# Kernel optimization log

Hardware: AMD Instinct MI355X
Metric: run time of the kernel (lower is better)

## Reference

```python
import jax, jax.numpy as jnp
import numpy as np

N_NODES = 100000
N_EDGES = 1600000
IN_DIM = 64
HID = 128
N_CLASSES = 1
N_GRAPHS = 512


def _glorot(key, shape):
    fan_in, fan_out = shape[0], shape[1]
    lim = (6.0 / (fan_in + fan_out)) ** 0.5
    return jax.random.uniform(key, shape, jnp.float32, -lim, lim)


def setup_inputs() -> dict:
    key = jax.random.key(0)
    ks = jax.random.split(key, 10)
    x = jax.random.normal(ks[0], (N_NODES, IN_DIM), jnp.float32)
    edge_src = jax.random.randint(ks[1], (N_EDGES,), 0, N_NODES)
    edge_dst = jax.random.randint(ks[2], (N_EDGES,), 0, N_NODES)
    graph_ids = jnp.sort(jax.random.randint(ks[3], (N_NODES,), 0, N_GRAPHS))
    return {
        "x": x,
        "edge_src": edge_src,
        "edge_dst": edge_dst,
        "graph_ids": graph_ids,
        "W1": _glorot(ks[4], (IN_DIM, HID)),
        "b1": jnp.zeros((HID,), jnp.float32),
        "W2": _glorot(ks[5], (HID, HID)),
        "b2": jnp.zeros((HID,), jnp.float32),
        "Wc1": _glorot(ks[6], (HID, HID)),
        "bc1": jnp.zeros((HID,), jnp.float32),
        "Wc2": _glorot(ks[7], (HID, HID)),
        "bc2": jnp.zeros((HID,), jnp.float32),
        "Wc3": _glorot(ks[8], (HID, N_CLASSES)),
        "bc3": jnp.zeros((N_CLASSES,), jnp.float32),
    }


def _graph_conv(h, edge_src, edge_dst, W, b):
    # DGL GraphConv, norm='both': out = D_out^{-1/2} A D_in^{-1/2} h W + b
    ones = jnp.ones((edge_src.shape[0],), h.dtype)
    deg_out = jnp.clip(jax.ops.segment_sum(ones, edge_src, num_segments=N_NODES), 1.0)
    deg_in = jnp.clip(jax.ops.segment_sum(ones, edge_dst, num_segments=N_NODES), 1.0)
    h = h * jax.lax.rsqrt(deg_out)[:, None]           # src-side norm
    agg = jax.ops.segment_sum(h[edge_src], edge_dst, num_segments=N_NODES)  # [N, D]
    agg = agg * jax.lax.rsqrt(deg_in)[:, None]        # dst-side norm
    return agg @ W + b


def reference(x, edge_src, edge_dst, graph_ids, W1, b1, W2, b2, Wc1, bc1, Wc2, bc2, Wc3, bc3):
    h = jax.nn.relu(_graph_conv(x, edge_src, edge_dst, W1, b1))
    h = jax.nn.relu(_graph_conv(h, edge_src, edge_dst, W2, b2))
    # mean_nodes pooling over batched graphs
    sums = jax.ops.segment_sum(h, graph_ids, num_segments=N_GRAPHS)  # [G, H]
    cnts = jax.ops.segment_sum(jnp.ones((N_NODES,), h.dtype), graph_ids, num_segments=N_GRAPHS)
    hg = sums / jnp.clip(cnts, 1.0)[:, None]
    out = jax.nn.relu(hg @ Wc1 + bc1)
    out = jax.nn.relu(out @ Wc2 + bc2)
    return out @ Wc3 + bc3  # [G, n_classes]
```

## Files before the change

### kernel.cpp

```cpp
#include <hip/hip_runtime.h>

#define N_NODES 100000
#define N_EDGES 1600000
#define IN_DIM 64
#define HID 128
#define N_GRAPHS 512
#define NBUCK 391

__global__ __launch_bounds__(256) void k_bhist(const int* __restrict__ src, const int* __restrict__ dst,
                                               int* __restrict__ dcnt, int* __restrict__ scnt) {
    __shared__ int hd[NBUCK];
    __shared__ int hs[NBUCK];
    const int t = threadIdx.x;
    const int e0 = blockIdx.x * 4096 + t * 16;
    for (int i = t; i < NBUCK; i += 256) { hd[i] = 0; hs[i] = 0; }
    __syncthreads();
    if (e0 < N_EDGES) {
        const int4* d4 = (const int4*)(dst + e0);
        const int4* s4 = (const int4*)(src + e0);
#pragma unroll
        for (int u = 0; u < 4; ++u) {
            int4 d = d4[u], s = s4[u];
            atomicAdd(&hd[d.x >> 8], 1); atomicAdd(&hd[d.y >> 8], 1);
            atomicAdd(&hd[d.z >> 8], 1); atomicAdd(&hd[d.w >> 8], 1);
            atomicAdd(&hs[s.x >> 8], 1); atomicAdd(&hs[s.y >> 8], 1);
            atomicAdd(&hs[s.z >> 8], 1); atomicAdd(&hs[s.w >> 8], 1);
        }
    }
    __syncthreads();
    for (int i = t; i < NBUCK; i += 256) {
        if (hd[i]) atomicAdd(&dcnt[i], hd[i]);
        if (hs[i]) atomicAdd(&scnt[i], hs[i]);
    }
}

__global__ __launch_bounds__(512) void k_bscan3(const int* __restrict__ dcnt, const int* __restrict__ scnt,
                                                const int* __restrict__ gid,
                                                int* __restrict__ dbase, int* __restrict__ sbase,
                                                int* __restrict__ dcur, int* __restrict__ scur,
                                                int* __restrict__ gstart) {
    const int t = threadIdx.x;
    if (blockIdx.x == 2) {
        for (int g = t; g <= N_GRAPHS; g += 512) {
            int lo = 0, hi = N_NODES;
            while (lo < hi) {
                int mid = (lo + hi) >> 1;
                if (gid[mid] < g) lo = mid + 1; else hi = mid;
            }
            gstart[g] = lo;
        }
        return;
    }
    __shared__ int l[512];
    const int* cntp = (blockIdx.x == 0) ? dcnt : scnt;
    int* basep = (blockIdx.x == 0) ? dbase : sbase;
    int* curp  = (blockIdx.x == 0) ? dcur  : scur;
    int v = (t < NBUCK) ? cntp[t] : 0;
    l[t] = v;
    __syncthreads();
    for (int off = 1; off < 512; off <<= 1) {
        int x = (t >= off) ? l[t - off] : 0;
        __syncthreads();
        l[t] += x;
        __syncthreads();
    }
    if (t < NBUCK) {
        int excl = l[t] - v;
        basep[t] = excl; curp[t] = excl;
    }
    if (t == NBUCK - 1) basep[NBUCK] = l[t];
}

__global__ __launch_bounds__(256) void k_bin2(const int* __restrict__ src, const int* __restrict__ dst,
                                              int* __restrict__ dcur, int* __restrict__ scur,
                                              int* __restrict__ binnedD, int* __restrict__ binnedS) {
    __shared__ int hd[NBUCK];
    __shared__ int bd[NBUCK];
    __shared__ int hs[NBUCK];
    __shared__ int bs[NBUCK];
    const int t = threadIdx.x;
    const int e0 = blockIdx.x * 4096 + t * 16;
    for (int i = t; i < NBUCK; i += 256) { hd[i] = 0; hs[i] = 0; }
    __syncthreads();
    if (e0 < N_EDGES) {
        const int4* d4 = (const int4*)(dst + e0);
        const int4* s4 = (const int4*)(src + e0);
#pragma unroll
        for (int u = 0; u < 4; ++u) {
            int4 d = d4[u], s = s4[u];
            atomicAdd(&hd[d.x >> 8], 1); atomicAdd(&hd[d.y >> 8], 1);
            atomicAdd(&hd[d.z >> 8], 1); atomicAdd(&hd[d.w >> 8], 1);
            atomicAdd(&hs[s.x >> 8], 1); atomicAdd(&hs[s.y >> 8], 1);
            atomicAdd(&hs[s.z >> 8], 1); atomicAdd(&hs[s.w >> 8], 1);
        }
    }
    __syncthreads();
    for (int i = t; i < NBUCK; i += 256) {
        int c = hd[i];
        bd[i] = c ? atomicAdd(&dcur[i], c) : 0;
        hd[i] = 0;
        c = hs[i];
        bs[i] = c ? atomicAdd(&scur[i], c) : 0;
        hs[i] = 0;
    }
    __syncthreads();
    if (e0 < N_EDGES) {
        const int4* d4 = (const int4*)(dst + e0);
        const int4* s4 = (const int4*)(src + e0);
#pragma unroll
        for (int u = 0; u < 4; ++u) {
            int4 d = d4[u];
            int4 s = s4[u];
            int bk, r;
            bk = d.x >> 8; r = atomicAdd(&hd[bk], 1); binnedD[bd[bk] + r] = s.x | ((d.x & 255) << 17);
            bk = d.y >> 8; r = atomicAdd(&hd[bk], 1); binnedD[bd[bk] + r] = s.y | ((d.y & 255) << 17);
            bk = d.z >> 8; r = atomicAdd(&hd[bk], 1); binnedD[bd[bk] + r] = s.z | ((d.z & 255) << 17);
            bk = d.w >> 8; r = atomicAdd(&hd[bk], 1); binnedD[bd[bk] + r] = s.w | ((d.w & 255) << 17);
            bk = s.x >> 8; r = atomicAdd(&hs[bk], 1); binnedS[bs[bk] + r] = s.x;
            bk = s.y >> 8; r = atomicAdd(&hs[bk], 1); binnedS[bs[bk] + r] = s.y;
            bk = s.z >> 8; r = atomicAdd(&hs[bk], 1); binnedS[bs[bk] + r] = s.z;
            bk = s.w >> 8; r = atomicAdd(&hs[bk], 1); binnedS[bs[bk] + r] = s.w;
        }
    }
}

__global__ __launch_bounds__(256) void k_prep2(const int* __restrict__ dbase, const int* __restrict__ sbase,
                                               const int* __restrict__ binnedD, const int* __restrict__ binnedS,
                                               int* __restrict__ rowp, float* __restrict__ rsi,
                                               float* __restrict__ rso, int* __restrict__ col) {
    const int t = threadIdx.x;
    if (blockIdx.x < NBUCK) {
        const int b = blockIdx.x;
        const int n0 = b * 256;
        __shared__ int cnt[256];
        __shared__ int scn[256];
        __shared__ int cur[256];
        __shared__ int sb[2];
        if (t < 2) sb[t] = dbase[b + t];
        cnt[t] = 0;
        __syncthreads();
        const int s = sb[0], e = sb[1];
        for (int i = s + t; i < e; i += 256) atomicAdd(&cnt[binnedD[i] >> 17], 1);
        __syncthreads();
        const int c = cnt[t];
        scn[t] = c;
        __syncthreads();
        for (int off = 1; off < 256; off <<= 1) {
            int v = (t >= off) ? scn[t - off] : 0;
            __syncthreads();
            scn[t] += v;
            __syncthreads();
        }
        const int excl = scn[t] - c;
        cur[t] = excl;
        if (n0 + t < N_NODES) {
            rowp[n0 + t] = s + excl;
            rsi[n0 + t] = 1.0f / sqrtf(fmaxf((float)c, 1.0f));
        }
        if (b == NBUCK - 1 && t == 0) rowp[N_NODES] = e;
        __syncthreads();
        for (int i = s + t; i < e; i += 256) {
            int p = binnedD[i];
            int r = atomicAdd(&cur[p >> 17], 1);
            col[s + r] = p & 0x1FFFF;
        }
    } else {
        const int b = blockIdx.x - NBUCK;
        const int n0 = b * 256;
        __shared__ int cnt2[256];
        __shared__ int sb2[2];
        if (t < 2) sb2[t] = sbase[b + t];
        cnt2[t] = 0;
        __syncthreads();
        const int s = sb2[0], e = sb2[1];
        for (int i = s + t; i < e; i += 256) atomicAdd(&cnt2[binnedS[i] - n0], 1);
        __syncthreads();
        if (n0 + t < N_NODES) rso[n0 + t] = 1.0f / sqrtf(fmaxf((float)cnt2[t], 1.0f));
    }
}

__global__ __launch_bounds__(512, 8) void k_g64mm(const float4* __restrict__ x4, const float* __restrict__ rso,
                                                  const int* __restrict__ rowp, const int* __restrict__ col,
                                                  const float* __restrict__ W, const float* __restrict__ bias,
                                                  const float* __restrict__ rsi, float* __restrict__ out) {
    __shared__ float aggL[32][IN_DIM];
    __shared__ float WL[32 * 128];
    const int t = threadIdx.x;
    const int wid = t >> 6, lane = t & 63;
    const int n0 = blockIdx.x * 32;

    const int grp = lane >> 4, li = lane & 15;
#pragma unroll 1
    for (int it = 0; it < 4; ++it) {
        const int node = n0 + wid * 4 + it;
        const int s = rowp[node], e = rowp[node + 1];
        float ax = 0.f, ay = 0.f, az = 0.f, aw = 0.f;
        int i = s + grp;
        for (; i + 12 < e; i += 16) {
            int c0 = col[i], c1 = col[i + 4], c2 = col[i + 8], c3 = col[i + 12];
            float4 v0 = x4[c0 * 16 + li];
            float4 v1 = x4[c1 * 16 + li];
            float4 v2 = x4[c2 * 16 + li];
            float4 v3 = x4[c3 * 16 + li];
            float r0 = rso[c0], r1 = rso[c1], r2 = rso[c2], r3 = rso[c3];
            ax = fmaf(r0, v0.x, ax); ay = fmaf(r0, v0.y, ay); az = fmaf(r0, v0.z, az); aw = fmaf(r0, v0.w, aw);
            ax = fmaf(r1, v1.x, ax); ay = fmaf(r1, v1.y, ay); az = fmaf(r1, v1.z, az); aw = fmaf(r1, v1.w, aw);
            ax = fmaf(r2, v2.x, ax); ay = fmaf(r2, v2.y, ay); az = fmaf(r2, v2.z, az); aw = fmaf(r2, v2.w, aw);
            ax = fmaf(r3, v3.x, ax); ay = fmaf(r3, v3.y, ay); az = fmaf(r3, v3.z, az); aw = fmaf(r3, v3.w, aw);
        }
        for (; i + 4 < e; i += 8) {
            int c0 = col[i], c1 = col[i + 4];
            float4 v0 = x4[c0 * 16 + li];
            float4 v1 = x4[c1 * 16 + li];
            float r0 = rso[c0], r1 = rso[c1];
            ax = fmaf(r0, v0.x, ax); ay = fmaf(r0, v0.y, ay); az = fmaf(r0, v0.z, az); aw = fmaf(r0, v0.w, aw);
            ax = fmaf(r1, v1.x, ax); ay = fmaf(r1, v1.y, ay); az = fmaf(r1, v1.z, az); aw = fmaf(r1, v1.w, aw);
        }
        for (; i < e; i += 4) {
            int c = col[i];
            float4 v = x4[c * 16 + li];
            float r = rso[c];
            ax = fmaf(r, v.x, ax); ay = fmaf(r, v.y, ay); az = fmaf(r, v.z, az); aw = fmaf(r, v.w, aw);
        }
        ax += __shfl_xor(ax, 16, 64); ay += __shfl_xor(ay, 16, 64);
        az += __shfl_xor(az, 16, 64); aw += __shfl_xor(aw, 16, 64);
        ax += __shfl_xor(ax, 32, 64); ay += __shfl_xor(ay, 32, 64);
        az += __shfl_xor(az, 32, 64); aw += __shfl_xor(aw, 32, 64);
        if (lane < 16) {
            float4 o; o.x = ax; o.y = ay; o.z = az; o.w = aw;
            ((float4*)aggL[node - n0])[li] = o;
        }
    }

    const int jq = t & 31;
    const int ns = t >> 5;
    float acc[2][4] = {};
    for (int kc = 0; kc < IN_DIM; kc += 32) {
        const float4* Wg = (const float4*)(W + kc * 128);
        float4* WL4 = (float4*)WL;
        __syncthreads();
#pragma unroll
        for (int u = 0; u < 2; ++u) WL4[t + 512 * u] = Wg[t + 512 * u];
        __syncthreads();
#pragma unroll
        for (int k = 0; k < 32; ++k) {
            float4 wv = ((const float4*)WL)[k * 32 + jq];
            float a0 = aggL[ns * 2 + 0][kc + k];
            float a1 = aggL[ns * 2 + 1][kc + k];
            acc[0][0] += a0 * wv.x; acc[0][1] += a0 * wv.y; acc[0][2] += a0 * wv.z; acc[0][3] += a0 * wv.w;
            acc[1][0] += a1 * wv.x; acc[1][1] += a1 * wv.y; acc[1][2] += a1 * wv.z; acc[1][3] += a1 * wv.w;
        }
    }
    float4 bj = ((const float4*)bias)[jq];
#pragma unroll
    for (int i = 0; i < 2; ++i) {
        int node = n0 + ns * 2 + i;
        float ri = rsi[node];
        float ro = rso[node];
        float4 o;
        o.x = fmaxf(acc[i][0] * ri + bj.x, 0.f) * ro;
        o.y = fmaxf(acc[i][1] * ri + bj.y, 0.f) * ro;
        o.z = fmaxf(acc[i][2] * ri + bj.z, 0.f) * ro;
        o.w = fmaxf(acc[i][3] * ri + bj.w, 0.f) * ro;
        *(float4*)(out + (size_t)node * HID + jq * 4) = o;
    }
}

__global__ __launch_bounds__(512, 8) void k_g128p(const float4* __restrict__ h4, const int* __restrict__ rowp,
                                                  const int* __restrict__ col, const float* __restrict__ W,
                                                  const float* __restrict__ bias, const float* __restrict__ rsi,
                                                  const int* __restrict__ gid, float* __restrict__ gsum,
                                                  float* __restrict__ partials) {
    __shared__ float agg[32][HID];
    __shared__ float WL[32 * 128];
    __shared__ float gpart[4][128];
    const int t = threadIdx.x;
    const int wid = t >> 6, lane = t & 63;
    const int n0 = blockIdx.x * 32;
    if (t < 512) ((float*)gpart)[t] = 0.f;

    const int grp = lane >> 5, li = lane & 31;
#pragma unroll 1
    for (int it = 0; it < 4; ++it) {
        const int node = n0 + wid * 4 + it;
        const int s = rowp[node], e = rowp[node + 1];
        float ax = 0.f, ay = 0.f, az = 0.f, aw = 0.f;
        int i = s + grp;
        for (; i + 6 < e; i += 8) {
            int c0 = col[i], c1 = col[i + 2], c2 = col[i + 4], c3 = col[i + 6];
            float4 v0 = h4[c0 * 32 + li];
            float4 v1 = h4[c1 * 32 + li];
            float4 v2 = h4[c2 * 32 + li];
            float4 v3 = h4[c3 * 32 + li];
            ax += v0.x + v1.x + v2.x + v3.x;
            ay += v0.y + v1.y + v2.y + v3.y;
            az += v0.z + v1.z + v2.z + v3.z;
            aw += v0.w + v1.w + v2.w + v3.w;
        }
        for (; i < e; i += 2) {
            float4 v = h4[col[i] * 32 + li];
            ax += v.x; ay += v.y; az += v.z; aw += v.w;
        }
        ax += __shfl_xor(ax, 32, 64); ay += __shfl_xor(ay, 32, 64);
        az += __shfl_xor(az, 32, 64); aw += __shfl_xor(aw, 32, 64);
        if (lane < 32) {
            float4 o; o.x = ax; o.y = ay; o.z = az; o.w = aw;
            ((float4*)agg[node - n0])[li] = o;
        }
    }

    const int jq = t & 31;
    const int ns = t >> 5;
    float acc[2][4] = {};
    for (int kc = 0; kc < HID; kc += 32) {
        const float4* Wg = (const float4*)(W + kc * 128);
        float4* WL4 = (float4*)WL;
        __syncthreads();
#pragma unroll
        for (int u = 0; u < 2; ++u) WL4[t + 512 * u] = Wg[t + 512 * u];
        __syncthreads();
#pragma unroll
        for (int k = 0; k < 32; ++k) {
            float4 wv = ((const float4*)WL)[k * 32 + jq];
            float a0 = agg[ns * 2 + 0][kc + k];
            float a1 = agg[ns * 2 + 1][kc + k];
            acc[0][0] += a0 * wv.x; acc[0][1] += a0 * wv.y; acc[0][2] += a0 * wv.z; acc[0][3] += a0 * wv.w;
            acc[1][0] += a1 * wv.x; acc[1][1] += a1 * wv.y; acc[1][2] += a1 * wv.z; acc[1][3] += a1 * wv.w;
        }
    }

    const int g0 = gid[n0];
    float4 bj = ((const float4*)bias)[jq];
    int curslot = -9;
    float p0 = 0.f, p1 = 0.f, p2 = 0.f, p3 = 0.f;
#pragma unroll
    for (int i = 0; i < 2; ++i) {
        int node = n0 + ns * 2 + i;
        float ri = rsi[node];
        float ox = fmaxf(acc[i][0] * ri + bj.x, 0.f);
        float oy = fmaxf(acc[i][1] * ri + bj.y, 0.f);
        float oz = fmaxf(acc[i][2] * ri + bj.z, 0.f);
        float ow = fmaxf(acc[i][3] * ri + bj.w, 0.f);
        int slot = gid[node] - g0;
        if (slot != curslot) {
            if (curslot >= 0) {
                if (curslot < 4) {
                    atomicAdd(&gpart[curslot][jq * 4 + 0], p0);
                    atomicAdd(&gpart[curslot][jq * 4 + 1], p1);
                    atomicAdd(&gpart[curslot][jq * 4 + 2], p2);
                    atomicAdd(&gpart[curslot][jq * 4 + 3], p3);
                } else {
                    atomicAdd(&gsum[(g0 + curslot) * HID + jq * 4 + 0], p0);
                    atomicAdd(&gsum[(g0 + curslot) * HID + jq * 4 + 1], p1);
                    atomicAdd(&gsum[(g0 + curslot) * HID + jq * 4 + 2], p2);
                    atomicAdd(&gsum[(g0 + curslot) * HID + jq * 4 + 3], p3);
                }
            }
            curslot = slot; p0 = ox; p1 = oy; p2 = oz; p3 = ow;
        } else {
            p0 += ox; p1 += oy; p2 += oz; p3 += ow;
        }
    }
    if (curslot >= 0) {
        if (curslot < 4) {
            atomicAdd(&gpart[curslot][jq * 4 + 0], p0);
            atomicAdd(&gpart[curslot][jq * 4 + 1], p1);
            atomicAdd(&gpart[curslot][jq * 4 + 2], p2);
            atomicAdd(&gpart[curslot][jq * 4 + 3], p3);
        } else {
            atomicAdd(&gsum[(g0 + curslot) * HID + jq * 4 + 0], p0);
            atomicAdd(&gsum[(g0 + curslot) * HID + jq * 4 + 1], p1);
            atomicAdd(&gsum[(g0 + curslot) * HID + jq * 4 + 2], p2);
            atomicAdd(&gsum[(g0 + curslot) * HID + jq * 4 + 3], p3);
        }
    }
    __syncthreads();
    if (t < 512) partials[(size_t)blockIdx.x * 512 + t] = ((float*)gpart)[t];
}

__global__ __launch_bounds__(128) void k_pool(const float* __restrict__ partials, const int* __restrict__ gid,
                                              const int* __restrict__ gstart, float* __restrict__ gsum) {
    const int g = blockIdx.x, t = threadIdx.x;
    const int s = gstart[g], e = gstart[g + 1];
    float sum = gsum[g * HID + t];
    if (e > s) {
        const int b0 = s >> 5, b1 = (e - 1) >> 5;
        for (int b = b0; b <= b1; ++b) {
            int sl = g - gid[b << 5];
            if (sl >= 0 && sl < 4) sum += partials[(size_t)b * 512 + sl * 128 + t];
        }
    }
    gsum[g * HID + t] = sum;
}

__global__ __launch_bounds__(128) void k_head(const float* __restrict__ gsum, const int* __restrict__ gstart,
                                              const float* __restrict__ Wc1, const float* __restrict__ bc1,
                                              const float* __restrict__ Wc2, const float* __restrict__ bc2,
                                              const float* __restrict__ Wc3, const float* __restrict__ bc3,
                                              float* __restrict__ out) {
    int g = blockIdx.x, t = threadIdx.x;
    int s = gstart[g], e = gstart[g + 1];
    float cnt = fmaxf((float)(e - s), 1.0f);
    __shared__ float buf[HID];
    __shared__ float red[2];
    buf[t] = gsum[g * HID + t] / cnt;
    __syncthreads();
    float a = bc1[t];
#pragma unroll 8
    for (int k = 0; k < HID; ++k) a += buf[k] * Wc1[k * HID + t];
    a = fmaxf(a, 0.f);
    __syncthreads();
    buf[t] = a;
    __syncthreads();
    float b = bc2[t];
#pragma unroll 8
    for (int k = 0; k < HID; ++k) b += buf[k] * Wc2[k * HID + t];
    b = fmaxf(b, 0.f);
    float p = b * Wc3[t];
    for (int off = 32; off > 0; off >>= 1) p += __shfl_down(p, off, 64);
    if ((t & 63) == 0) red[t >> 6] = p;
    __syncthreads();
    if (t == 0) out[g] = red[0] + red[1] + bc3[0];
}

extern "C" void kernel_launch(void* const* d_in, const int* in_sizes, int n_in,
                              void* d_out, int out_size, void* d_ws, size_t ws_size,
                              hipStream_t stream) {
    const float* x   = (const float*)d_in[0];
    const int* esrc  = (const int*)d_in[1];
    const int* edst  = (const int*)d_in[2];
    const int* gid   = (const int*)d_in[3];
    const float* W1  = (const float*)d_in[4];
    const float* b1  = (const float*)d_in[5];
    const float* W2  = (const float*)d_in[6];
    const float* b2  = (const float*)d_in[7];
    const float* Wc1 = (const float*)d_in[8];
    const float* bc1 = (const float*)d_in[9];
    const float* Wc2 = (const float*)d_in[10];
    const float* bc2 = (const float*)d_in[11];
    const float* Wc3 = (const float*)d_in[12];
    const float* bc3 = (const float*)d_in[13];
    float* out = (float*)d_out;

    char* w = (char*)d_ws;
    size_t off = 0;
    auto alloc = [&](size_t bytes) -> char* {
        char* p = w + off;
        off += (bytes + 255) & ~(size_t)255;
        return p;
    };
    int* dcnt   = (int*)alloc((size_t)2 * (NBUCK + 1) * 4);
    int* scnt   = dcnt + (NBUCK + 1);
    int* dbase  = (int*)alloc((size_t)(NBUCK + 1) * 4);
    int* sbase  = (int*)alloc((size_t)(NBUCK + 1) * 4);
    int* dcur   = (int*)alloc((size_t)NBUCK * 4);
    int* scur   = (int*)alloc((size_t)NBUCK * 4);
    float* rso  = (float*)alloc((size_t)N_NODES * 4);
    float* rsi  = (float*)alloc((size_t)N_NODES * 4);
    int* rowp   = (int*)alloc((size_t)(N_NODES + 1) * 4);
    int* gstart = (int*)alloc((size_t)(N_GRAPHS + 1) * 4);
    int* col    = (int*)alloc((size_t)N_EDGES * 4);
    float* gsum = (float*)alloc((size_t)N_GRAPHS * HID * 4);
    float* R1   = (float*)alloc((size_t)N_NODES * HID * 4);
    float* R2   = (float*)alloc((size_t)N_NODES * HID * 4);
    int* binnedD = (int*)R1;
    int* binnedS = (int*)R1 + (size_t)N_EDGES;
    float* partials = R1;
    float* h1s  = R2;

    (void)in_sizes; (void)n_in; (void)out_size; (void)ws_size;

    hipMemsetAsync(dcnt, 0, (size_t)2 * (NBUCK + 1) * 4, stream);
    hipMemsetAsync(gsum, 0, (size_t)N_GRAPHS * HID * 4, stream);

    const int BB = (N_EDGES + 4095) / 4096;
    const int FB32 = N_NODES / 32;

    k_bhist<<<BB, 256, 0, stream>>>(esrc, edst, dcnt, scnt);
    k_bscan3<<<3, 512, 0, stream>>>(dcnt, scnt, gid, dbase, sbase, dcur, scur, gstart);
    k_bin2<<<BB, 256, 0, stream>>>(esrc, edst, dcur, scur, binnedD, binnedS);
    k_prep2<<<2 * NBUCK, 256, 0, stream>>>(dbase, sbase, binnedD, binnedS, rowp, rsi, rso, col);
    k_g64mm<<<FB32, 512, 0, stream>>>((const float4*)x, rso, rowp, col, W1, b1, rsi, h1s);
    k_g128p<<<FB32, 512, 0, stream>>>((const float4*)h1s, rowp, col, W2, b2, rsi, gid, gsum, partials);
    k_pool<<<N_GRAPHS, 128, 0, stream>>>(partials, gid, gstart, gsum);
    k_head<<<N_GRAPHS, 128, 0, stream>>>(gsum, gstart, Wc1, bc1, Wc2, bc2, Wc3, bc3, out);
}
```

Baseline: 330.6 us.

## Split layer-2 gather from matmul+pooling into separate kernels

Unfuses the second GraphConv layer. A standalone wave-per-node gather kernel with a deeper 8-way unroll writes the aggregated features to global memory, and a separate tiled matmul kernel (64 nodes per block, 8 rows per thread) applies W2, bias, ReLU and the graph pooling partials. The intent is to give the gather higher occupancy and more loads in flight, and to give the matmul better register reuse. The cost is an extra 51 MB round trip through global memory for the aggregated activations and one more kernel launch. The pool kernel's block indexing is updated to match the new 64-node block size.

```diff
diff --git a/kernel.cpp b/kernel.cpp
--- a/kernel.cpp
+++ b/kernel.cpp
@@ -266,76 +266,106 @@
     }
 }
 
-__global__ __launch_bounds__(512, 8) void k_g128p(const float4* __restrict__ h4, const int* __restrict__ rowp,
-                                                  const int* __restrict__ col, const float* __restrict__ W,
-                                                  const float* __restrict__ bias, const float* __restrict__ rsi,
-                                                  const int* __restrict__ gid, float* __restrict__ gsum,
-                                                  float* __restrict__ partials) {
-    __shared__ float agg[32][HID];
+__global__ __launch_bounds__(256) void k_gather128(const float4* __restrict__ h4, const int* __restrict__ rowp,
+                                                   const int* __restrict__ col, float4* __restrict__ agg4) {
+    int wv = (blockIdx.x * 256 + threadIdx.x) >> 6;
+    if (wv >= N_NODES) return;
+    int lane = threadIdx.x & 63;
+    int grp = lane >> 5, li = lane & 31;
+    int s = rowp[wv], e = rowp[wv + 1];
+    float ax = 0.f, ay = 0.f, az = 0.f, aw = 0.f;
+    int i = s + grp;
+    for (; i + 14 < e; i += 16) {
+        int c0 = col[i],      c1 = col[i + 2],  c2 = col[i + 4],  c3 = col[i + 6];
+        int c4 = col[i + 8],  c5 = col[i + 10], c6 = col[i + 12], c7 = col[i + 14];
+        float4 v0 = h4[c0 * 32 + li];
+        float4 v1 = h4[c1 * 32 + li];
+        float4 v2 = h4[c2 * 32 + li];
+        float4 v3 = h4[c3 * 32 + li];
+        float4 v4 = h4[c4 * 32 + li];
+        float4 v5 = h4[c5 * 32 + li];
+        float4 v6 = h4[c6 * 32 + li];
+        float4 v7 = h4[c7 * 32 + li];
+        ax += (v0.x + v1.x) + (v2.x + v3.x) + ((v4.x + v5.x) + (v6.x + v7.x));
+        ay += (v0.y + v1.y) + (v2.y + v3.y) + ((v4.y + v5.y) + (v6.y + v7.y));
+        az += (v0.z + v1.z) + (v2.z + v3.z) + ((v4.z + v5.z) + (v6.z + v7.z));
+        aw += (v0.w + v1.w) + (v2.w + v3.w) + ((v4.w + v5.w) + (v6.w + v7.w));
+    }
+    for (; i + 6 < e; i += 8) {
+        int c0 = col[i], c1 = col[i + 2], c2 = col[i + 4], c3 = col[i + 6];
+        float4 v0 = h4[c0 * 32 + li];
+        float4 v1 = h4[c1 * 32 + li];
+        float4 v2 = h4[c2 * 32 + li];
+        float4 v3 = h4[c3 * 32 + li];
+        ax += v0.x + v1.x + v2.x + v3.x;
+        ay += v0.y + v1.y + v2.y + v3.y;
+        az += v0.z + v1.z + v2.z + v3.z;
+        aw += v0.w + v1.w + v2.w + v3.w;
+    }
+    for (; i < e; i += 2) {
+        float4 v = h4[col[i] * 32 + li];
+        ax += v.x; ay += v.y; az += v.z; aw += v.w;
+    }
+    ax += __shfl_xor(ax, 32, 64); ay += __shfl_xor(ay, 32, 64);
+    az += __shfl_xor(az, 32, 64); aw += __shfl_xor(aw, 32, 64);
+    if (lane < 32) {
+        float4 o; o.x = ax; o.y = ay; o.z = az; o.w = aw;
+        agg4[wv * 32 + li] = o;
+    }
+}
+
+__global__ __launch_bounds__(256) void k_mm2p(const float* __restrict__ A, const float* __restrict__ W,
+                                              const float* __restrict__ bias, const float* __restrict__ rsi,
+                                              const int* __restrict__ gid, float* __restrict__ gsum,
+                                              float* __restrict__ partials) {
     __shared__ float WL[32 * 128];
+    __shared__ float aL[64][33];
     __shared__ float gpart[4][128];
     const int t = threadIdx.x;
-    const int wid = t >> 6, lane = t & 63;
-    const int n0 = blockIdx.x * 32;
-    if (t < 512) ((float*)gpart)[t] = 0.f;
-
-    const int grp = lane >> 5, li = lane & 31;
-#pragma unroll 1
-    for (int it = 0; it < 4; ++it) {
-        const int node = n0 + wid * 4 + it;
-        const int s = rowp[node], e = rowp[node + 1];
-        float ax = 0.f, ay = 0.f, az = 0.f, aw = 0.f;
-        int i = s + grp;
-        for (; i + 6 < e; i += 8) {
-            int c0 = col[i], c1 = col[i + 2], c2 = col[i + 4], c3 = col[i + 6];
-            float4 v0 = h4[c0 * 32 + li];
-            float4 v1 = h4[c1 * 32 + li];
-            float4 v2 = h4[c2 * 32 + li];
-            float4 v3 = h4[c3 * 32 + li];
-            ax += v0.x + v1.x + v2.x + v3.x;
-            ay += v0.y + v1.y + v2.y + v3.y;
-            az += v0.z + v1.z + v2.z + v3.z;
-            aw += v0.w + v1.w + v2.w + v3.w;
-        }
-        for (; i < e; i += 2) {
-            float4 v = h4[col[i] * 32 + li];
-            ax += v.x; ay += v.y; az += v.z; aw += v.w;
-        }
-        ax += __shfl_xor(ax, 32, 64); ay += __shfl_xor(ay, 32, 64);
-        az += __shfl_xor(az, 32, 64); aw += __shfl_xor(aw, 32, 64);
-        if (lane < 32) {
-            float4 o; o.x = ax; o.y = ay; o.z = az; o.w = aw;
-            ((float4*)agg[node - n0])[li] = o;
-        }
-    }
-
     const int jq = t & 31;
     const int ns = t >> 5;
-    float acc[2][4] = {};
+    const int n0 = blockIdx.x * 64;
+    for (int u = t; u < 512; u += 256) ((float*)gpart)[u] = 0.f;
+    float acc[8][4] = {};
     for (int kc = 0; kc < HID; kc += 32) {
         const float4* Wg = (const float4*)(W + kc * 128);
         float4* WL4 = (float4*)WL;
         __syncthreads();
 #pragma unroll
-        for (int u = 0; u < 2; ++u) WL4[t + 512 * u] = Wg[t + 512 * u];
+        for (int u = 0; u < 4; ++u) WL4[t + 256 * u] = Wg[t + 256 * u];
+        {
+            int r = t >> 2, q = t & 3;
+            int node = n0 + r;
+#pragma unroll
+            for (int h = 0; h < 2; ++h) {
+                int qq = q + h * 4;
+                float4 v = make_float4(0.f, 0.f, 0.f, 0.f);
+                if (node < N_NODES) v = *(const float4*)(A + (size_t)node * HID + kc + qq * 4);
+                aL[r][qq * 4 + 0] = v.x; aL[r][qq * 4 + 1] = v.y;
+                aL[r][qq * 4 + 2] = v.z; aL[r][qq * 4 + 3] = v.w;
+            }
+        }
         __syncthreads();
 #pragma unroll
         for (int k = 0; k < 32; ++k) {
             float4 wv = ((const float4*)WL)[k * 32 + jq];
-            float a0 = agg[ns * 2 + 0][kc + k];
-            float a1 = agg[ns * 2 + 1][kc + k];
-            acc[0][0] += a0 * wv.x; acc[0][1] += a0 * wv.y; acc[0][2] += a0 * wv.z; acc[0][3] += a0 * wv.w;
-            acc[1][0] += a1 * wv.x; acc[1][1] += a1 * wv.y; acc[1][2] += a1 * wv.z; acc[1][3] += a1 * wv.w;
-        }
-    }
-
+#pragma unroll
+            for (int i = 0; i < 8; ++i) {
+                float av = aL[ns * 8 + i][k];
+                acc[i][0] += av * wv.x; acc[i][1] += av * wv.y;
+                acc[i][2] += av * wv.z; acc[i][3] += av * wv.w;
+            }
+        }
+    }
+    __syncthreads();
     const int g0 = gid[n0];
     float4 bj = ((const float4*)bias)[jq];
     int curslot = -9;
     float p0 = 0.f, p1 = 0.f, p2 = 0.f, p3 = 0.f;
 #pragma unroll
-    for (int i = 0; i < 2; ++i) {
-        int node = n0 + ns * 2 + i;
+    for (int i = 0; i < 8; ++i) {
+        int node = n0 + ns * 8 + i;
+        if (node >= N_NODES) break;
         float ri = rsi[node];
         float ox = fmaxf(acc[i][0] * ri + bj.x, 0.f);
         float oy = fmaxf(acc[i][1] * ri + bj.y, 0.f);
@@ -375,7 +405,7 @@
         }
     }
     __syncthreads();
-    if (t < 512) partials[(size_t)blockIdx.x * 512 + t] = ((float*)gpart)[t];
+    for (int u = t; u < 512; u += 256) partials[(size_t)blockIdx.x * 512 + u] = ((float*)gpart)[u];
 }
 
 __global__ __launch_bounds__(128) void k_pool(const float* __restrict__ partials, const int* __restrict__ gid,
@@ -384,9 +414,9 @@
     const int s = gstart[g], e = gstart[g + 1];
     float sum = gsum[g * HID + t];
     if (e > s) {
-        const int b0 = s >> 5, b1 = (e - 1) >> 5;
+        const int b0 = s >> 6, b1 = (e - 1) >> 6;
         for (int b = b0; b <= b1; ++b) {
-            int sl = g - gid[b << 5];
+            int sl = g - gid[b << 6];
             if (sl >= 0 && sl < 4) sum += partials[(size_t)b * 512 + sl * 128 + t];
         }
     }
@@ -461,11 +491,12 @@
     int* gstart = (int*)alloc((size_t)(N_GRAPHS + 1) * 4);
     int* col    = (int*)alloc((size_t)N_EDGES * 4);
     float* gsum = (float*)alloc((size_t)N_GRAPHS * HID * 4);
+    float* partials = (float*)alloc((size_t)1563 * 512 * 4);
     float* R1   = (float*)alloc((size_t)N_NODES * HID * 4);
     float* R2   = (float*)alloc((size_t)N_NODES * HID * 4);
     int* binnedD = (int*)R1;
     int* binnedS = (int*)R1 + (size_t)N_EDGES;
-    float* partials = R1;
+    float* agg2 = R1;
     float* h1s  = R2;
 
     (void)in_sizes; (void)n_in; (void)out_size; (void)ws_size;
@@ -475,13 +506,16 @@
 
     const int BB = (N_EDGES + 4095) / 4096;
     const int FB32 = N_NODES / 32;
+    const int GB = (N_NODES * 64 + 255) / 256;
+    const int MB64 = (N_NODES + 63) / 64;
 
     k_bhist<<<BB, 256, 0, stream>>>(esrc, edst, dcnt, scnt);
     k_bscan3<<<3, 512, 0, stream>>>(dcnt, scnt, gid, dbase, sbase, dcur, scur, gstart);
     k_bin2<<<BB, 256, 0, stream>>>(esrc, edst, dcur, scur, binnedD, binnedS);
     k_prep2<<<2 * NBUCK, 256, 0, stream>>>(dbase, sbase, binnedD, binnedS, rowp, rsi, rso, col);
     k_g64mm<<<FB32, 512, 0, stream>>>((const float4*)x, rso, rowp, col, W1, b1, rsi, h1s);
-    k_g128p<<<FB32, 512, 0, stream>>>((const float4*)h1s, rowp, col, W2, b2, rsi, gid, gsum, partials);
+    k_gather128<<<GB, 256, 0, stream>>>((const float4*)h1s, rowp, col, (float4*)agg2);
+    k_mm2p<<<MB64, 256, 0, stream>>>(agg2, W2, b2, rsi, gid, gsum, partials);
     k_pool<<<N_GRAPHS, 128, 0, stream>>>(partials, gid, gstart, gsum);
     k_head<<<N_GRAPHS, 128, 0, stream>>>(gsum, gstart, Wc1, bc1, Wc2, bc2, Wc3, bc3, out);
 }
```

Measured after the change: 349.3 us. +5.7%, slower.
